# Performance work log

Measured on AMD Instinct MI355X. Metric: run time of the kernel, lower is better.

## Reference

```python
import jax, jax.numpy as jnp
import numpy as np

_K_MASK = float(jnp.finfo(jnp.float32).min)
EPS = 1e-6
B, T, D = 2, 2048, 2048
NH, NKV, HD = 16, 4, 128


def _rope_tables(key):
    # Standard RoPE tables: (B, T, HD) with [freqs, freqs] layout (rotate_half convention)
    inv_freq = 1.0 / (10000.0 ** (np.arange(0, HD, 2, dtype=np.float32) / HD))  # (HD/2,)
    pos = np.arange(T, dtype=np.float32)
    freqs = np.einsum('t,f->tf', pos, inv_freq)              # (T, HD/2)
    emb = np.concatenate([freqs, freqs], axis=-1)            # (T, HD)
    cos = jnp.broadcast_to(jnp.cos(emb)[None], (B, T, HD))
    sin = jnp.broadcast_to(jnp.sin(emb)[None], (B, T, HD))
    return cos, sin


def setup_inputs() -> dict:
    key = jax.random.key(0)
    ks = jax.random.split(key, 6)
    s = 0.02
    cos, sin = _rope_tables(key)
    return {
        'x': jax.random.normal(ks[0], (B, T, D), jnp.float32),
        'cos': cos,
        'sin': sin,
        'wq': jax.random.normal(ks[1], (D, NH * HD * 2), jnp.float32) * s,
        'wk': jax.random.normal(ks[2], (D, NKV * HD), jnp.float32) * s,
        'wv': jax.random.normal(ks[3], (D, NKV * HD), jnp.float32) * s,
        'wo': jax.random.normal(ks[4], (NH * HD, D), jnp.float32) * s,
        'q_norm_w': jnp.ones((HD,), jnp.float32),
        'k_norm_w': jnp.ones((HD,), jnp.float32),
        'segment_ids': jnp.ones((B, T), jnp.int32),
        'position_ids': jnp.broadcast_to(jnp.arange(T, dtype=jnp.int32)[None], (B, T)),
    }


def _rmsnorm(x, w):
    var = jnp.mean(jnp.square(x.astype(jnp.float32)), axis=-1, keepdims=True)
    return (x.astype(jnp.float32) * jax.lax.rsqrt(var + EPS)).astype(x.dtype) * w


def _rotate_half(x):
    x1, x2 = jnp.split(x, 2, axis=-1)
    return jnp.concatenate([-x2, x1], axis=-1)


def _apply_rope(q, k, cos, sin):
    # q: (B, NH, T, HD), k: (B, NKV, T, HD), cos/sin: (B, T, HD)
    c = cos[:, None, :, :]
    s = sin[:, None, :, :]
    q = q * c + _rotate_half(q) * s
    k = k * c + _rotate_half(k) * s
    return q, k


def reference(x, cos, sin, wq, wk, wv, wo, q_norm_w, k_norm_w, segment_ids, position_ids):
    Bx, Tx, _ = x.shape
    n_rep = NH // NKV
    scale = HD ** -0.5

    q_out = (x @ wq).reshape(Bx, Tx, NH, HD * 2)
    query, gate = jnp.split(q_out, 2, axis=-1)         # each (B, T, NH, HD)
    gate = gate.reshape(Bx, Tx, -1)                    # (B, T, NH*HD)
    query = _rmsnorm(query, q_norm_w).transpose(0, 2, 1, 3)   # (B, NH, T, HD)
    key = _rmsnorm((x @ wk).reshape(Bx, Tx, NKV, HD), k_norm_w).transpose(0, 2, 1, 3)
    value = (x @ wv).reshape(Bx, Tx, NKV, HD).transpose(0, 2, 1, 3)

    query, key = _apply_rope(query, key, cos, sin)
    if n_rep > 1:
        key = jnp.repeat(key, n_rep, axis=1)
        value = jnp.repeat(value, n_rep, axis=1)

    attn_logits = jnp.einsum('bhqd,bhkd->bhqk', query, key) * scale
    causal = position_ids[:, :, None] >= position_ids[:, None, :]
    seg = segment_ids[:, :, None] == segment_ids[:, None, :]
    mask = (causal & seg)[:, None, :, :]
    attn_logits = jnp.where(mask, attn_logits, _K_MASK)
    attn_weights = jax.nn.softmax(attn_logits.astype(jnp.float32), axis=-1).astype(attn_logits.dtype)
    attn_out = jnp.einsum('bhqk,bhkd->bhqd', attn_weights, value)
    attn_out = attn_out.transpose(0, 2, 1, 3).reshape(Bx, Tx, -1)  # (B, T, NH*HD)
    attn_out = attn_out * jax.nn.sigmoid(gate)
    return attn_out @ wo
```

## Files before the change

### kernel.cpp

```cpp
#include <hip/hip_runtime.h>

#define AS1 __attribute__((address_space(1)))
#define AS3 __attribute__((address_space(3)))

typedef __bf16 bf16x8 __attribute__((ext_vector_type(8)));
typedef float f32x4 __attribute__((ext_vector_type(4)));
typedef float f32x16 __attribute__((ext_vector_type(16)));
typedef unsigned short us8 __attribute__((ext_vector_type(8)));
typedef unsigned int u32x4 __attribute__((ext_vector_type(4)));

static constexpr int T_ = 2048;
static constexpr int NH_ = 16;
static constexpr int NKV_ = 4;
static constexpr int HD_ = 128;
static constexpr int NQKV_ = 5120;
static constexpr float SL2E_ = 0.12751744f;

static __device__ __forceinline__ unsigned short f2b(float f) {
  unsigned u = __builtin_bit_cast(unsigned, f);
  u += 0x7fffu + ((u >> 16) & 1u);
  return (unsigned short)(u >> 16);
}
static __device__ __forceinline__ void load_lds16(const void* g, void* l) {
  __builtin_amdgcn_global_load_lds((const AS1 unsigned int*)g, (AS3 unsigned int*)l, 16, 0, 0);
}
static __device__ __forceinline__ f32x4 mfma16(bf16x8 a, bf16x8 b, f32x4 c) {
  return __builtin_amdgcn_mfma_f32_16x16x32_bf16(a, b, c, 0, 0, 0);
}
static __device__ __forceinline__ f32x16 mfma32(bf16x8 a, bf16x8 b, f32x16 c) {
  return __builtin_amdgcn_mfma_f32_32x32x16_bf16(a, b, c, 0, 0, 0);
}
static __device__ __forceinline__ unsigned cvtpk(float lo, float hi) {
  unsigned r;
  asm("v_cvt_pk_bf16_f32 %0, %1, %2" : "=v"(r) : "v"(lo), "v"(hi));
  return r;
}
static __device__ __forceinline__ void pl32swap(unsigned& a, unsigned& b) {
  asm("v_permlane32_swap_b32 %0, %1" : "+v"(a), "+v"(b));
}
#define S_BARRIER() asm volatile("s_barrier" ::: "memory")

__global__ __launch_bounds__(256) void conv_bf16_kernel(
    const float* __restrict__ src, unsigned short* __restrict__ dst, int n) {
  int i = (blockIdx.x * 256 + threadIdx.x) * 4;
  if (i >= n) return;
  float4 v = *(const float4*)(src + i);
  ushort4 o;
  o.x = f2b(v.x); o.y = f2b(v.y); o.z = f2b(v.z); o.w = f2b(v.w);
  *(ushort4*)(dst + i) = o;
}

__global__ void tconv_kernel(const float* __restrict__ src, unsigned short* __restrict__ dst,
                             int R, int C, int roff) {
  __shared__ float tile[32][33];
  const int c0 = blockIdx.x * 32, r0 = blockIdx.y * 32;
#pragma unroll
  for (int j = 0; j < 32; j += 8)
    tile[threadIdx.y + j][threadIdx.x] =
        src[(size_t)(r0 + threadIdx.y + j) * C + c0 + threadIdx.x];
  __syncthreads();
#pragma unroll
  for (int j = 0; j < 32; j += 8)
    dst[(size_t)(roff + c0 + threadIdx.y + j) * R + r0 + threadIdx.x] =
        f2b(tile[threadIdx.x][threadIdx.y + j]);
}

__global__ void vtrans_kernel(const float* __restrict__ qkv, unsigned short* __restrict__ Vt) {
  __shared__ unsigned short tile[32][33];
  const int bh = blockIdx.z;
  const int b = bh >> 2, vh = bh & 3;
  const int d0 = blockIdx.x * 32, t0 = blockIdx.y * 32;
#pragma unroll
  for (int j = 0; j < 32; j += 8) {
    const int t = t0 + threadIdx.y + j;
    tile[threadIdx.y + j][threadIdx.x] =
        f2b(qkv[(size_t)(b * T_ + t) * NQKV_ + 4608 + vh * 128 + d0 + threadIdx.x]);
  }
  __syncthreads();
  unsigned short* dst = Vt + (size_t)bh * HD_ * T_;
#pragma unroll
  for (int j = 0; j < 32; j += 8)
    dst[(size_t)(d0 + threadIdx.y + j) * T_ + t0 + threadIdx.x] =
        tile[threadIdx.x][threadIdx.y + j];
}

__global__ __launch_bounds__(512, 2) void gemm_bt8_kernel(
    const unsigned short* __restrict__ A, const unsigned short* __restrict__ Bt,
    float* __restrict__ C, int K, int N) {
  __shared__ __align__(16) unsigned short As[3][128 * 64];
  __shared__ __align__(16) unsigned short Bs[3][256 * 64];
  const int tid = threadIdx.x;
  const int wid = tid >> 6, lane = tid & 63;
  const int lq = lane & 15, lg = lane >> 4;
  const int l8 = lane >> 3, s8 = lane & 7;
  const int wr = wid >> 2, wc = wid & 3;
  const int brow = blockIdx.y * 128, bcol = blockIdx.x * 256;

  f32x4 acc[4][4];
#pragma unroll
  for (int m = 0; m < 4; ++m)
#pragma unroll
    for (int n = 0; n < 4; ++n) acc[m][n] = (f32x4){0.f, 0.f, 0.f, 0.f};

  auto STAGE_HALF = [&](int t, int b3t, int half) {
    const int k0 = t * 64;
    {
      const int ca = wid + half * 8;
      const int row = ca * 8 + l8;
      load_lds16(A + (size_t)(brow + row) * K + k0 + ((s8 ^ (row & 7)) << 3),
                 &As[b3t][ca << 9]);
    }
#pragma unroll
    for (int j = 0; j < 2; ++j) {
      const int cb = wid + half * 16 + (j << 3);
      const int row = cb * 8 + l8;
      load_lds16(Bt + (size_t)(bcol + row) * K + k0 + ((s8 ^ (row & 7)) << 3),
                 &Bs[b3t][cb << 9]);
    }
  };
  auto PHASE_READS = [&](int b3, int ks, bf16x8* a, bf16x8* bb) {
#pragma unroll
    for (int m = 0; m < 4; ++m) {
      const int r = wr * 64 + m * 16 + lq;
      a[m] = *(const bf16x8*)&As[b3][r * 64 + (((ks * 4 + lg) ^ (r & 7)) << 3)];
    }
#pragma unroll
    for (int n = 0; n < 4; ++n) {
      const int r = wc * 64 + n * 16 + lq;
      bb[n] = *(const bf16x8*)&Bs[b3][r * 64 + (((ks * 4 + lg) ^ (r & 7)) << 3)];
    }
  };
  auto DO_MFMA = [&](bf16x8* a, bf16x8* bb) {
    __builtin_amdgcn_s_setprio(1);
#pragma unroll
    for (int m = 0; m < 4; ++m)
#pragma unroll
      for (int n = 0; n < 4; ++n) acc[m][n] = mfma16(a[m], bb[n], acc[m][n]);
    __builtin_amdgcn_s_setprio(0);
  };

  STAGE_HALF(0, 0, 0); STAGE_HALF(0, 0, 1);
  STAGE_HALF(1, 1, 0); STAGE_HALF(1, 1, 1);
  asm volatile("s_waitcnt vmcnt(6)" ::: "memory");
  S_BARRIER();

  int b3 = 0;
  for (int t = 0; t < 32; ++t) {
    const int b3p2 = b3 < 1 ? b3 + 2 : b3 - 1;
    bf16x8 a[4], bb[4];
    PHASE_READS(b3, 0, a, bb);
    if (t < 30) STAGE_HALF(t + 2, b3p2, 0);
    S_BARRIER();
    __builtin_amdgcn_sched_barrier(0);
    DO_MFMA(a, bb);
    S_BARRIER();
    PHASE_READS(b3, 1, a, bb);
    if (t < 30) STAGE_HALF(t + 2, b3p2, 1);
    if (t < 30) {
      asm volatile("s_waitcnt vmcnt(6)" ::: "memory");
    } else if (t == 30) {
      asm volatile("s_waitcnt vmcnt(0)" ::: "memory");
    }
    S_BARRIER();
    __builtin_amdgcn_sched_barrier(0);
    DO_MFMA(a, bb);
    if (t < 31) S_BARRIER();
    b3 = b3 < 2 ? b3 + 1 : 0;
  }
#pragma unroll
  for (int m = 0; m < 4; ++m)
#pragma unroll
    for (int n = 0; n < 4; ++n)
#pragma unroll
      for (int r = 0; r < 4; ++r)
        C[(size_t)(brow + wr * 64 + m * 16 + lg * 4 + r) * N + bcol + wc * 64 + n * 16 + lq] =
            acc[m][n][r];
}

__global__ __launch_bounds__(256) void postproc_kernel(
    const float* __restrict__ qkv, const float* __restrict__ cosT,
    const float* __restrict__ sinT, const float* __restrict__ qnw,
    const float* __restrict__ knw, unsigned short* __restrict__ Qg,
    unsigned short* __restrict__ Kg) {
  const int row = blockIdx.x;
  const int b = row >> 11, t = row & 2047;
  const float* src = qkv + (size_t)row * NQKV_;
  const int tid = threadIdx.x;
  const int sub = tid & 15;
  const int i0 = sub * 8;
  const bool lo = sub < 8;

  float cs[8], sn[8];
#pragma unroll
  for (int j = 0; j < 8; ++j) {
    cs[j] = cosT[(size_t)row * HD_ + i0 + j];
    sn[j] = sinT[(size_t)row * HD_ + i0 + j];
  }
  {
    const int h = tid >> 4;
    float q[8], ss = 0.f;
#pragma unroll
    for (int j = 0; j < 8; ++j) { q[j] = src[h * 256 + i0 + j]; ss += q[j] * q[j]; }
    ss += __shfl_xor(ss, 1); ss += __shfl_xor(ss, 2);
    ss += __shfl_xor(ss, 4); ss += __shfl_xor(ss, 8);
    const float rms = rsqrtf(ss * (1.f / 128.f) + 1e-6f);
    float qn[8];
#pragma unroll
    for (int j = 0; j < 8; ++j) qn[j] = q[j] * rms * qnw[i0 + j];
    float pr[8];
#pragma unroll
    for (int j = 0; j < 8; ++j) pr[j] = __shfl_xor(qn[j], 8);
    us8 ov;
#pragma unroll
    for (int j = 0; j < 8; ++j) ov[j] = f2b(qn[j] * cs[j] + (lo ? -pr[j] : pr[j]) * sn[j]);
    *(us8*)(Qg + ((size_t)(b * NH_ + h) * T_ + t) * HD_ + i0) = ov;
  }
  if (tid < 64) {
    const int kh = tid >> 4;
    float k[8], ss = 0.f;
#pragma unroll
    for (int j = 0; j < 8; ++j) { k[j] = src[4096 + kh * 128 + i0 + j]; ss += k[j] * k[j]; }
    ss += __shfl_xor(ss, 1); ss += __shfl_xor(ss, 2);
    ss += __shfl_xor(ss, 4); ss += __shfl_xor(ss, 8);
    const float rms = rsqrtf(ss * (1.f / 128.f) + 1e-6f);
    float kn[8];
#pragma unroll
    for (int j = 0; j < 8; ++j) kn[j] = k[j] * rms * knw[i0 + j];
    float pr[8];
#pragma unroll
    for (int j = 0; j < 8; ++j) pr[j] = __shfl_xor(kn[j], 8);
    us8 ov;
#pragma unroll
    for (int j = 0; j < 8; ++j) ov[j] = f2b(kn[j] * cs[j] + (lo ? -pr[j] : pr[j]) * sn[j]);
    *(us8*)(Kg + ((size_t)(b * NKV_ + kh) * T_ + t) * HD_ + i0) = ov;
  }
}

__global__ __launch_bounds__(256, 2) void attn_kernel(
    const unsigned short* __restrict__ Qg, const unsigned short* __restrict__ Kg,
    const unsigned short* __restrict__ Vt, const float* __restrict__ qkv,
    unsigned short* __restrict__ attnb) {
  __shared__ __align__(16) char smem[65536];
  const int i = blockIdx.x;
  const int xi = (i >> 3) & 15;
  const int grp = (i & 7) + ((i >> 7) << 3);
  const int h = grp & 15, b = grp >> 4;
  const int qt = b ? (15 - xi) : xi;
  const int kh = h >> 2;
  const int tid = threadIdx.x, wid = tid >> 6, lane = tid & 63;
  const int lq = lane & 31, hi = lane >> 5;
  const int q0 = qt * 128;
  const int qbase = q0 + wid * 32;
  const int qrow = qbase + lq;

  bf16x8 qf[8];
  const unsigned short* qptr = Qg + ((size_t)(b * NH_ + h) * T_ + qrow) * HD_;
#pragma unroll
  for (int t = 0; t < 8; ++t) qf[t] = *(const bf16x8*)(qptr + t * 16 + hi * 8);

  const char* Kbase = (const char*)(Kg + (size_t)(b * NKV_ + kh) * T_ * HD_);
  const char* Vbase = (const char*)(Vt + (size_t)(b * NKV_ + kh) * HD_ * T_);

  f32x16 o[4];
#pragma unroll
  for (int d = 0; d < 4; ++d)
#pragma unroll
    for (int r = 0; r < 16; ++r) o[d][r] = 0.f;
  float m_r = -1e30f, l_r = 0.f;
  const int nt = 2 * qt + 2;

  auto STAGE = [&](int tt, int c) {
    const int t0 = tt * 64;
    char* kd = smem + c * 32768;
    char* vd = kd + 16384;
#pragma unroll
    for (int j = 0; j < 4; ++j) {
      const int ch = j * 4 + wid;
      const int kv = ch * 4 + (lane >> 4);
      load_lds16(Kbase + (size_t)(t0 + kv) * 256 + (((lane & 15) ^ (kv & 7)) << 4),
                 kd + ch * 1024);
      const int dv = ch * 8 + (lane >> 3);
      load_lds16(Vbase + (size_t)dv * (T_ * 2) + (size_t)t0 * 2 +
                     (((lane & 7) ^ (dv & 7)) << 4),
                 vd + ch * 1024);
    }
  };

  STAGE(0, 0);
  __syncthreads();
  int cur = 0;
  for (int tt = 0; tt < nt; ++tt) {
    const int t0 = tt * 64;
    if (tt + 1 < nt) STAGE(tt + 1, cur ^ 1);
    if (t0 <= qbase + 31) {
      const char* kd = smem + cur * 32768;
      const char* vd = kd + 16384;
      f32x16 sA, sB;
#pragma unroll
      for (int r = 0; r < 16; ++r) { sA[r] = 0.f; sB[r] = 0.f; }
      __builtin_amdgcn_s_setprio(1);
#pragma unroll
      for (int t = 0; t < 8; ++t) {
        const int sw = t * 2 + hi;
        bf16x8 ka = *(const bf16x8*)(kd + lq * 256 + ((sw ^ (lq & 7)) << 4));
        bf16x8 kb = *(const bf16x8*)(kd + (lq + 32) * 256 + ((sw ^ (lq & 7)) << 4));
        sA = mfma32(ka, qf[t], sA);
        sB = mfma32(kb, qf[t], sB);
      }
      __builtin_amdgcn_s_setprio(0);
      float p[32];
      float mx = -1e30f;
      const bool anymask = (t0 + 63 > qbase);
#pragma unroll
      for (int r = 0; r < 16; ++r) {
        const int kv = (r & 3) + ((r >> 2) << 3) + hi * 4;
        float vA = sA[r] * SL2E_;
        float vB = sB[r] * SL2E_;
        if (anymask) {
          if (t0 + kv > qrow) vA = -1e30f;
          if (t0 + kv + 32 > qrow) vB = -1e30f;
        }
        p[r] = vA; p[16 + r] = vB;
        mx = fmaxf(mx, fmaxf(vA, vB));
      }
      mx = fmaxf(mx, __shfl_xor(mx, 32));
      const float mn = fmaxf(m_r, mx);
      const float al = exp2f(m_r - mn);
      float sum = 0.f;
#pragma unroll
      for (int j = 0; j < 32; ++j) { p[j] = exp2f(p[j] - mn); sum += p[j]; }
      sum += __shfl_xor(sum, 32);
      l_r = l_r * al + sum;
      m_r = mn;
#pragma unroll
      for (int d = 0; d < 4; ++d)
#pragma unroll
        for (int r = 0; r < 16; ++r) o[d][r] *= al;
      bf16x8 pf[4];
#pragma unroll
      for (int kt = 0; kt < 4; ++kt) {
        const float* pp = p + kt * 8;
        unsigned a0 = cvtpk(pp[0], pp[1]);
        unsigned a1 = cvtpk(pp[2], pp[3]);
        unsigned b0 = cvtpk(pp[4], pp[5]);
        unsigned b1 = cvtpk(pp[6], pp[7]);
        pl32swap(a0, b0);
        pl32swap(a1, b1);
        u32x4 w = {a0, a1, b0, b1};
        pf[kt] = __builtin_bit_cast(bf16x8, w);
      }
      __builtin_amdgcn_s_setprio(1);
#pragma unroll
      for (int dt = 0; dt < 4; ++dt) {
        const int d = dt * 32 + lq;
#pragma unroll
        for (int kt = 0; kt < 4; ++kt) {
          bf16x8 vf = *(const bf16x8*)(vd + d * 128 + (((kt * 2 + hi) ^ (d & 7)) << 4));
          o[dt] = mfma32(vf, pf[kt], o[dt]);
        }
      }
      __builtin_amdgcn_s_setprio(0);
    }
    __syncthreads();
    cur ^= 1;
  }
  const float inv = 1.f / l_r;
  const float* grow = qkv + (size_t)(b * T_ + qrow) * NQKV_ + h * 256 + 128;
  unsigned short* orow = attnb + (size_t)(b * T_ + qrow) * (NH_ * HD_) + h * HD_;
#pragma unroll
  for (int dt = 0; dt < 4; ++dt)
#pragma unroll
    for (int g = 0; g < 4; ++g) {
      const int d0 = dt * 32 + g * 8 + hi * 4;
      float4 gv = *(const float4*)(grow + d0);
      ushort4 ov;
      ov.x = f2b(o[dt][g * 4 + 0] * inv / (1.f + __expf(-gv.x)));
      ov.y = f2b(o[dt][g * 4 + 1] * inv / (1.f + __expf(-gv.y)));
      ov.z = f2b(o[dt][g * 4 + 2] * inv / (1.f + __expf(-gv.z)));
      ov.w = f2b(o[dt][g * 4 + 3] * inv / (1.f + __expf(-gv.w)));
      *(ushort4*)(orow + d0) = ov;
    }
}

extern "C" void kernel_launch(void* const* d_in, const int* in_sizes, int n_in,
                              void* d_out, int out_size, void* d_ws, size_t ws_size,
                              hipStream_t stream) {
  (void)in_sizes; (void)n_in; (void)out_size; (void)ws_size;
  const float* x    = (const float*)d_in[0];
  const float* cosT = (const float*)d_in[1];
  const float* sinT = (const float*)d_in[2];
  const float* wq   = (const float*)d_in[3];
  const float* wk   = (const float*)d_in[4];
  const float* wv   = (const float*)d_in[5];
  const float* wo   = (const float*)d_in[6];
  const float* qnw  = (const float*)d_in[7];
  const float* knw  = (const float*)d_in[8];
  float* out = (float*)d_out;
  char* ws = (char*)d_ws;

  constexpr size_t OFF_XB    = 0;
  constexpr size_t OFF_WQKVT = OFF_XB    + (size_t)4096 * 2048 * 2;
  constexpr size_t OFF_WOT   = OFF_WQKVT + (size_t)5120 * 2048 * 2;
  constexpr size_t OFF_QKV   = OFF_WOT   + (size_t)2048 * 2048 * 2;
  constexpr size_t OFF_QG    = OFF_QKV   + (size_t)4096 * 5120 * 4;
  constexpr size_t OFF_KG    = OFF_QG    + (size_t)2 * 16 * 2048 * 128 * 2;
  constexpr size_t OFF_VT    = OFF_KG    + (size_t)2 * 4 * 2048 * 128 * 2;
  constexpr size_t OFF_ATTNB = OFF_VT    + (size_t)2 * 4 * 128 * 2048 * 2;

  unsigned short* xb    = (unsigned short*)(ws + OFF_XB);
  unsigned short* wqkvT = (unsigned short*)(ws + OFF_WQKVT);
  unsigned short* woT   = (unsigned short*)(ws + OFF_WOT);
  float*          qkv   = (float*)(ws + OFF_QKV);
  unsigned short* Qg    = (unsigned short*)(ws + OFF_QG);
  unsigned short* Kg    = (unsigned short*)(ws + OFF_KG);
  unsigned short* Vt    = (unsigned short*)(ws + OFF_VT);
  unsigned short* attnb = (unsigned short*)(ws + OFF_ATTNB);

  const int nX = 4096 * 2048;
  conv_bf16_kernel<<<nX / 4 / 256, 256, 0, stream>>>(x, xb, nX);
  tconv_kernel<<<dim3(4096 / 32, 2048 / 32), dim3(32, 8), 0, stream>>>(wq, wqkvT, 2048, 4096, 0);
  tconv_kernel<<<dim3(512 / 32, 2048 / 32), dim3(32, 8), 0, stream>>>(wk, wqkvT, 2048, 512, 4096);
  tconv_kernel<<<dim3(512 / 32, 2048 / 32), dim3(32, 8), 0, stream>>>(wv, wqkvT, 2048, 512, 4608);
  tconv_kernel<<<dim3(2048 / 32, 2048 / 32), dim3(32, 8), 0, stream>>>(wo, woT, 2048, 2048, 0);

  gemm_bt8_kernel<<<dim3(5120 / 256, 4096 / 128), 512, 0, stream>>>(xb, wqkvT, qkv, 2048, 5120);

  postproc_kernel<<<4096, 256, 0, stream>>>(qkv, cosT, sinT, qnw, knw, Qg, Kg);
  vtrans_kernel<<<dim3(128 / 32, 2048 / 32, 8), dim3(32, 8), 0, stream>>>(qkv, Vt);

  attn_kernel<<<512, 256, 0, stream>>>(Qg, Kg, Vt, qkv, attnb);

  gemm_bt8_kernel<<<dim3(2048 / 256, 4096 / 128), 512, 0, stream>>>(attnb, woT, out, 2048, 2048);
}
```

Before: 277.7 us.

## Add 256x256-tile GEMM with quadrant-split pipelining for QKV projection

Adds a new bf16 GEMM kernel with 256x256 output tiles per 512-thread block and uses it for the QKV projection. It double-buffers 64-wide K slices, splits each iteration into four MFMA quadrants with loads of the next slices between them, uses setprio around the MFMA bursts, and remaps block IDs in an XCD-aware order. The larger tile roughly doubles the arithmetic done per byte loaded compared with the 128x256 kernel, but it uses 128 KB of LDS and many accumulator registers. The grid drops to 320 blocks, which may hurt load balance across CUs.

```diff
diff --git a/kernel.cpp b/kernel.cpp
--- a/kernel.cpp
+++ b/kernel.cpp
@@ -82,6 +82,144 @@
   for (int j = 0; j < 32; j += 8)
     dst[(size_t)(d0 + threadIdx.y + j) * T_ + t0 + threadIdx.x] =
         tile[threadIdx.x][threadIdx.y + j];
+}
+
+__global__ __launch_bounds__(512, 2) void gemm256_kernel(
+    const unsigned short* __restrict__ A, const unsigned short* __restrict__ Bt,
+    float* __restrict__ C, int K, int N) {
+  __shared__ __align__(16) unsigned short As[2][256 * 64];
+  __shared__ __align__(16) unsigned short Bs[2][256 * 64];
+  const int gw = N >> 8;
+  const int nwg = gridDim.x;
+  int bid = blockIdx.x;
+  bid = (bid & 7) * (nwg >> 3) + (bid >> 3);
+  const int brow = (bid / gw) * 256, bcol = (bid % gw) * 256;
+
+  const int tid = threadIdx.x;
+  const int wid = tid >> 6, lane = tid & 63;
+  const int lq = lane & 15, lg = lane >> 4;
+  const int wr = wid >> 2, wc = wid & 3;
+
+  f32x4 acc[8][4];
+#pragma unroll
+  for (int m = 0; m < 8; ++m)
+#pragma unroll
+    for (int n = 0; n < 4; ++n) acc[m][n] = (f32x4){0.f, 0.f, 0.f, 0.f};
+
+  auto STAGE2 = [&](const unsigned short* __restrict__ M, int brc, int t,
+                    unsigned short* buf, int half) {
+    const int k0 = t * 64;
+#pragma unroll
+    for (int j = 0; j < 2; ++j) {
+      const int ch = half * 16 + j * 8 + wid;
+      const int row = ch * 8 + (lane >> 3);
+      load_lds16(M + (size_t)(brc + row) * K + k0 + (((lane & 7) ^ (row & 7)) << 3),
+                 buf + (ch << 9));
+    }
+  };
+  auto RD_A = [&](int p, int m, int ks) -> bf16x8 {
+    const int r = wr * 128 + m * 16 + lq;
+    return *(const bf16x8*)&As[p][r * 64 + (((ks * 4 + lg) ^ (r & 7)) << 3)];
+  };
+  auto RD_B = [&](int p, int n, int ks) -> bf16x8 {
+    const int r = wc * 64 + n * 16 + lq;
+    return *(const bf16x8*)&Bs[p][r * 64 + (((ks * 4 + lg) ^ (r & 7)) << 3)];
+  };
+
+  STAGE2(A, brow, 0, &As[0][0], 0);  STAGE2(A, brow, 0, &As[0][0], 1);
+  STAGE2(Bt, bcol, 0, &Bs[0][0], 0); STAGE2(Bt, bcol, 0, &Bs[0][0], 1);
+  STAGE2(Bt, bcol, 1, &Bs[1][0], 0); STAGE2(Bt, bcol, 1, &Bs[1][0], 1);
+  asm volatile("s_waitcnt vmcnt(4)" ::: "memory");
+  __builtin_amdgcn_s_barrier();
+
+  const int NT = K >> 6;
+  for (int t = 0; t < NT; ++t) {
+    const int p = t & 1;
+    unsigned short* Ab = &As[p ^ 1][0];
+    unsigned short* Bb = &Bs[p][0];
+    bf16x8 aL[4][2], aH[4][2], bL[2][2], bH[2][2];
+#pragma unroll
+    for (int m = 0; m < 4; ++m)
+#pragma unroll
+      for (int ks = 0; ks < 2; ++ks) aL[m][ks] = RD_A(p, m, ks);
+#pragma unroll
+    for (int n = 0; n < 2; ++n)
+#pragma unroll
+      for (int ks = 0; ks < 2; ++ks) bL[n][ks] = RD_B(p, n, ks);
+    if (t < NT - 1) STAGE2(A, brow, t + 1, Ab, 0);
+    __builtin_amdgcn_s_barrier();
+    __builtin_amdgcn_sched_barrier(0);
+    __builtin_amdgcn_s_setprio(1);
+#pragma unroll
+    for (int m = 0; m < 4; ++m)
+#pragma unroll
+      for (int n = 0; n < 2; ++n) {
+        acc[m][n] = mfma16(aL[m][0], bL[n][0], acc[m][n]);
+        acc[m][n] = mfma16(aL[m][1], bL[n][1], acc[m][n]);
+      }
+    __builtin_amdgcn_s_setprio(0);
+    __builtin_amdgcn_s_barrier();
+#pragma unroll
+    for (int n = 0; n < 2; ++n)
+#pragma unroll
+      for (int ks = 0; ks < 2; ++ks) bH[n][ks] = RD_B(p, n + 2, ks);
+    if (t < NT - 1) STAGE2(A, brow, t + 1, Ab, 1);
+    __builtin_amdgcn_s_barrier();
+    __builtin_amdgcn_sched_barrier(0);
+    __builtin_amdgcn_s_setprio(1);
+#pragma unroll
+    for (int m = 0; m < 4; ++m)
+#pragma unroll
+      for (int n = 0; n < 2; ++n) {
+        acc[m][n + 2] = mfma16(aL[m][0], bH[n][0], acc[m][n + 2]);
+        acc[m][n + 2] = mfma16(aL[m][1], bH[n][1], acc[m][n + 2]);
+      }
+    __builtin_amdgcn_s_setprio(0);
+    __builtin_amdgcn_s_barrier();
+#pragma unroll
+    for (int m = 0; m < 4; ++m)
+#pragma unroll
+      for (int ks = 0; ks < 2; ++ks) aH[m][ks] = RD_A(p, m + 4, ks);
+    if (t < NT - 2) STAGE2(Bt, bcol, t + 2, Bb, 0);
+    __builtin_amdgcn_s_barrier();
+    __builtin_amdgcn_sched_barrier(0);
+    __builtin_amdgcn_s_setprio(1);
+#pragma unroll
+    for (int m = 0; m < 4; ++m)
+#pragma unroll
+      for (int n = 0; n < 2; ++n) {
+        acc[m + 4][n + 2] = mfma16(aH[m][0], bH[n][0], acc[m + 4][n + 2]);
+        acc[m + 4][n + 2] = mfma16(aH[m][1], bH[n][1], acc[m + 4][n + 2]);
+      }
+    __builtin_amdgcn_s_setprio(0);
+    __builtin_amdgcn_s_barrier();
+    if (t < NT - 2) {
+      STAGE2(Bt, bcol, t + 2, Bb, 1);
+      asm volatile("s_waitcnt vmcnt(4)" ::: "memory");
+    } else if (t == NT - 2) {
+      asm volatile("s_waitcnt vmcnt(0)" ::: "memory");
+    }
+    __builtin_amdgcn_s_barrier();
+    __builtin_amdgcn_sched_barrier(0);
+    __builtin_amdgcn_s_setprio(1);
+#pragma unroll
+    for (int m = 0; m < 4; ++m)
+#pragma unroll
+      for (int n = 0; n < 2; ++n) {
+        acc[m + 4][n] = mfma16(aH[m][0], bL[n][0], acc[m + 4][n]);
+        acc[m + 4][n] = mfma16(aH[m][1], bL[n][1], acc[m + 4][n]);
+      }
+    __builtin_amdgcn_s_setprio(0);
+    __builtin_amdgcn_s_barrier();
+  }
+#pragma unroll
+  for (int m = 0; m < 8; ++m)
+#pragma unroll
+    for (int n = 0; n < 4; ++n)
+#pragma unroll
+      for (int r = 0; r < 4; ++r)
+        C[(size_t)(brow + wr * 128 + m * 16 + lg * 4 + r) * N + bcol + wc * 64 + n * 16 + lq] =
+            acc[m][n][r];
 }
 
 __global__ __launch_bounds__(512, 2) void gemm_bt8_kernel(
@@ -423,7 +561,7 @@
   tconv_kernel<<<dim3(512 / 32, 2048 / 32), dim3(32, 8), 0, stream>>>(wv, wqkvT, 2048, 512, 4608);
   tconv_kernel<<<dim3(2048 / 32, 2048 / 32), dim3(32, 8), 0, stream>>>(wo, woT, 2048, 2048, 0);
 
-  gemm_bt8_kernel<<<dim3(5120 / 256, 4096 / 128), 512, 0, stream>>>(xb, wqkvT, qkv, 2048, 5120);
+  gemm256_kernel<<<320, 512, 0, stream>>>(xb, wqkvT, qkv, 2048, 5120);
 
   postproc_kernel<<<4096, 256, 0, stream>>>(qkv, cosT, sinT, qnw, knw, Qg, Kg);
   vtrans_kernel<<<dim3(128 / 32, 2048 / 32, 8), dim3(32, 8), 0, stream>>>(qkv, Vt);
```

Measured after the change: 295.4 us. +6.3%, slower.
